# Kernel optimization log

Hardware: AMD Instinct MI355X
Metric: run time of the kernel (lower is better)

## Reference

```python
import jax, jax.numpy as jnp
import numpy as np

B, S, E, H, ML = 4, 1024, 1024, 16, 2048
HD = E // H


def setup_inputs() -> dict:
    key = jax.random.key(0)
    ks = jax.random.split(key, 8)
    s = 0.02
    return {
        "x": jax.random.normal(ks[0], (B, S, E), dtype=jnp.float32),
        "rel_pos": jax.random.normal(ks[1], (H, ML), dtype=jnp.float32),
        "in_proj_w": jax.random.normal(ks[2], (3 * E, E), dtype=jnp.float32) * s,
        "in_proj_b": jnp.zeros((3 * E,), jnp.float32),
        "out_w": jax.random.normal(ks[3], (E, E), dtype=jnp.float32) * s,
        "out_b": jnp.zeros((E,), jnp.float32),
        "w1": jax.random.normal(ks[4], (4 * E, E), dtype=jnp.float32) * s,
        "b1": jnp.zeros((4 * E,), jnp.float32),
        "w2": jax.random.normal(ks[5], (E, 4 * E), dtype=jnp.float32) * s,
        "b2": jnp.zeros((E,), jnp.float32),
        "ln1_g": jnp.ones((E,), jnp.float32),
        "ln1_b": jnp.zeros((E,), jnp.float32),
        "ln2_g": jnp.ones((E,), jnp.float32),
        "ln2_b": jnp.zeros((E,), jnp.float32),
    }


def _layernorm(x, g, b, eps=1e-5):
    m = x.mean(-1, keepdims=True)
    v = ((x - m) ** 2).mean(-1, keepdims=True)
    return (x - m) * jax.lax.rsqrt(v + eps) * g + b


def _causal_mask(size, rel_pos):
    # rel_pos: [H, max_len]; size <= max_len branch of the torch code
    flipped = jnp.flip(rel_pos[:, :size], -1)                        # [H, size]
    neg_inf = jnp.full((rel_pos.shape[0], size), -jnp.inf, rel_pos.dtype)
    padded = jnp.concatenate([flipped, neg_inf], axis=-1)            # [H, 2*size]
    idx = jnp.arange(size)[None, :] - jnp.arange(size)[:, None] + size - 1
    return padded[:, idx]                                            # [H, S, S]: rel_pos[i-j] if j<=i else -inf


def reference(x, rel_pos, in_proj_w, in_proj_b, out_w, out_b,
              w1, b1, w2, b2, ln1_g, ln1_b, ln2_g, ln2_b):
    b, s, e = x.shape
    xn = _layernorm(x, ln1_g, ln1_b)
    qkv = xn @ in_proj_w.T + in_proj_b                               # [B,S,3E]
    q, k, v = jnp.split(qkv, 3, axis=-1)
    q = q.reshape(b, s, H, HD).transpose(0, 2, 1, 3)                 # [B,H,S,D]
    k = k.reshape(b, s, H, HD).transpose(0, 2, 1, 3)
    v = v.reshape(b, s, H, HD).transpose(0, 2, 1, 3)
    mask = _causal_mask(s, rel_pos)                                  # [H,S,S], broadcast over batch (== repeat(B,1,1))
    scores = jnp.einsum("bhqd,bhkd->bhqk", q, k) / np.sqrt(HD) + mask[None]
    attn = jax.nn.softmax(scores, axis=-1)
    o = jnp.einsum("bhqk,bhkd->bhqd", attn, v)                       # [B,H,S,D]
    o = o.transpose(0, 2, 1, 3).reshape(b, s, e)
    att_out = o @ out_w.T + out_b
    x = x + att_out
    xm = _layernorm(x, ln2_g, ln2_b)
    mlp = jax.nn.relu(xm @ w1.T + b1) @ w2.T + b2
    return x + mlp
```

## Files before the change

kernel.cpp:

```cpp
#include <hip/hip_runtime.h>
#include <stdint.h>

typedef __bf16 bf16x8 __attribute__((ext_vector_type(8)));
typedef float  f32x4  __attribute__((ext_vector_type(4)));

__device__ __forceinline__ unsigned short f2bf(float f) {
  union { float f; unsigned int u; } a; a.f = f;
  unsigned int r = a.u + 0x7FFFu + ((a.u >> 16) & 1u);
  return (unsigned short)(r >> 16);
}

__device__ __forceinline__ unsigned short f2bf_fast(float f) {
  union { __bf16 b; unsigned short u; } v; v.b = (__bf16)f; return v.u;
}

__device__ __forceinline__ void cp16(const void* g, void* l) {
  auto g1 = reinterpret_cast<__attribute__((address_space(1))) unsigned int*>(
      reinterpret_cast<uintptr_t>(g));
  auto l3 = reinterpret_cast<__attribute__((address_space(3))) unsigned int*>(
      reinterpret_cast<uintptr_t>(l));
  __builtin_amdgcn_global_load_lds(g1, l3, 16, 0, 0);
}

__global__ __launch_bounds__(256) void cvt_all(
    const float* __restrict__ s0, const float* __restrict__ s1,
    const float* __restrict__ s2, const float* __restrict__ s3,
    unsigned short* __restrict__ d0, unsigned short* __restrict__ d1,
    unsigned short* __restrict__ d2, unsigned short* __restrict__ d3) {
  int i = (blockIdx.x * 256 + threadIdx.x) * 4;
  const float* src; unsigned short* dst; int off;
  if (i < 3145728)       { src = s0; dst = d0; off = 0; }
  else if (i < 4194304)  { src = s1; dst = d1; off = 3145728; }
  else if (i < 8388608)  { src = s2; dst = d2; off = 4194304; }
  else                   { src = s3; dst = d3; off = 8388608; }
  i -= off;
  float4 v = *(const float4*)(src + i);
  union { unsigned short u[4]; uint2 p; } o;
  o.u[0] = f2bf(v.x); o.u[1] = f2bf(v.y); o.u[2] = f2bf(v.z); o.u[3] = f2bf(v.w);
  *(uint2*)(dst + i) = o.p;
}

__global__ __launch_bounds__(256) void ln_bf16_seed(
    const float* __restrict__ x,
    const float* __restrict__ g,
    const float* __restrict__ bta,
    unsigned short* __restrict__ out,
    const float* __restrict__ seed_bias,
    float* __restrict__ seed_out) {
  const int row = blockIdx.x, t = threadIdx.x;
  const float4 v = *(const float4*)(x + (size_t)row * 1024 + t * 4);
  {
    float4 sb = *(const float4*)(seed_bias + t * 4);
    float4 sv;
    sv.x = v.x + sb.x; sv.y = v.y + sb.y; sv.z = v.z + sb.z; sv.w = v.w + sb.w;
    *(float4*)(seed_out + (size_t)row * 1024 + t * 4) = sv;
  }
  float s1 = v.x + v.y + v.z + v.w;
  float s2 = v.x*v.x + v.y*v.y + v.z*v.z + v.w*v.w;
  #pragma unroll
  for (int off = 1; off < 64; off <<= 1) {
    s1 += __shfl_xor(s1, off, 64);
    s2 += __shfl_xor(s2, off, 64);
  }
  __shared__ float r1[4], r2[4];
  if ((t & 63) == 0) { r1[t >> 6] = s1; r2[t >> 6] = s2; }
  __syncthreads();
  s1 = r1[0] + r1[1] + r1[2] + r1[3];
  s2 = r2[0] + r2[1] + r2[2] + r2[3];
  const float mean = s1 * (1.0f / 1024.0f);
  const float var  = s2 * (1.0f / 1024.0f) - mean * mean;
  const float rstd = rsqrtf(var + 1e-5f);
  const float4 gv = *(const float4*)(g + t * 4);
  const float4 bv = *(const float4*)(bta + t * 4);
  union { unsigned short u[4]; uint2 p; } o;
  o.u[0] = f2bf((v.x - mean) * rstd * gv.x + bv.x);
  o.u[1] = f2bf((v.y - mean) * rstd * gv.y + bv.y);
  o.u[2] = f2bf((v.z - mean) * rstd * gv.z + bv.z);
  o.u[3] = f2bf((v.w - mean) * rstd * gv.w + bv.w);
  *(uint2*)(out + (size_t)row * 1024 + t * 4) = o.p;
}

template <int MODE>
__device__ __forceinline__ void gemm_core(
    const unsigned short* __restrict__ A,
    const unsigned short* __restrict__ Bt,
    const float* __restrict__ bias,
    void* __restrict__ outp,
    int N, int K, int kbeg, int kend,
    unsigned short* As, unsigned short* Bs) {
  const int tid = threadIdx.x;
  const int wave = tid >> 6, lane = tid & 63;
  const int q = lane >> 4, c = lane & 15;
  const int wm = (wave & 1) << 6, wn = (wave >> 1) << 6;
  const int m0 = blockIdx.x << 7, n0 = blockIdx.y << 7;

  const int srow = tid >> 3;
  const int cg8  = ((tid & 7) ^ (srow & 7)) << 3;

  const unsigned short* gA = A  + (size_t)(m0 + srow) * K + cg8;
  const unsigned short* gB = Bt + (size_t)(n0 + srow) * K + cg8;
  const size_t rstep = (size_t)32 * K;

  auto issue = [&](int k0, int buf) {
    unsigned short* lA = As + buf * 8192 + tid * 8;
    unsigned short* lB = Bs + buf * 8192 + tid * 8;
    #pragma unroll
    for (int it = 0; it < 4; it++) {
      cp16(gA + it * rstep + k0, lA + it * 2048);
      cp16(gB + it * rstep + k0, lB + it * 2048);
    }
  };

  const f32x4 fzero = {0.f, 0.f, 0.f, 0.f};
  f32x4 acc[4][4];
  #pragma unroll
  for (int i = 0; i < 4; i++)
    #pragma unroll
    for (int j = 0; j < 4; j++) acc[i][j] = fzero;

  issue(kbeg, 0);
  if (kbeg + 64 < kend) issue(kbeg + 64, 1);

  int buf = 0;
  for (int k0 = kbeg; k0 < kend; k0 += 64, buf ^= 1) {
    if (k0 + 64 < kend) asm volatile("s_waitcnt vmcnt(8)" ::: "memory");
    else                asm volatile("s_waitcnt vmcnt(0)" ::: "memory");
    asm volatile("s_barrier" ::: "memory");

    const unsigned short* cA = As + buf * 8192;
    const unsigned short* cB = Bs + buf * 8192;
    #pragma unroll
    for (int ks = 0; ks < 2; ks++) {
      const int sw = (((ks << 2) + q) ^ (c & 7)) << 3;
      bf16x8 af[4], bf[4];
      #pragma unroll
      for (int i = 0; i < 4; i++) af[i] = *(const bf16x8*)&cA[(wm + i*16 + c)*64 + sw];
      #pragma unroll
      for (int j = 0; j < 4; j++) bf[j] = *(const bf16x8*)&cB[(wn + j*16 + c)*64 + sw];
      #pragma unroll
      for (int i = 0; i < 4; i++)
        #pragma unroll
        for (int j = 0; j < 4; j++)
          acc[i][j] = __builtin_amdgcn_mfma_f32_16x16x32_bf16(af[i], bf[j], acc[i][j], 0, 0, 0);
    }

    asm volatile("s_barrier" ::: "memory");
    if (k0 + 128 < kend) issue(k0 + 128, buf);
  }

  if (MODE == 4) {
    float* op = (float*)outp;
    #pragma unroll
    for (int i = 0; i < 4; i++) {
      #pragma unroll
      for (int r = 0; r < 4; r++) {
        const int row = m0 + wm + i * 16 + q * 4 + r;
        #pragma unroll
        for (int j = 0; j < 4; j++) {
          const int col = n0 + wn + j * 16 + c;
          atomicAdd(op + (size_t)row * N + col, acc[i][j][r]);
        }
      }
    }
  } else {
    float bj[4];
    #pragma unroll
    for (int j = 0; j < 4; j++) bj[j] = bias[n0 + wn + j * 16 + c];
    #pragma unroll
    for (int i = 0; i < 4; i++) {
      #pragma unroll
      for (int r = 0; r < 4; r++) {
        const int row = m0 + wm + i * 16 + q * 4 + r;
        #pragma unroll
        for (int j = 0; j < 4; j++) {
          const int col = n0 + wn + j * 16 + c;
          const size_t idx = (size_t)row * N + col;
          float v = acc[i][j][r] + bj[j];
          if (MODE == 0) ((unsigned short*)outp)[idx] = f2bf(v);
          else           ((unsigned short*)outp)[idx] = f2bf(fmaxf(v, 0.f));
        }
      }
    }
  }
}

template <int MODE>
__global__ __launch_bounds__(256, 2) void gemm_bt(
    const unsigned short* __restrict__ A,
    const unsigned short* __restrict__ Bt,
    const float* __restrict__ bias,
    void* __restrict__ outp,
    int N, int K) {
  __shared__ __align__(16) unsigned short As[2 * 128 * 64];
  __shared__ __align__(16) unsigned short Bs[2 * 128 * 64];
  gemm_core<MODE>(A, Bt, bias, outp, N, K, 0, K, As, Bs);
}

__global__ __launch_bounds__(256, 2) void gemm_bt_splitk(
    const unsigned short* __restrict__ A,
    const unsigned short* __restrict__ Bt,
    float* __restrict__ outp,
    int N, int K) {
  __shared__ __align__(16) unsigned short As[2 * 128 * 64];
  __shared__ __align__(16) unsigned short Bs[2 * 128 * 64];
  const int KH = K >> 1;
  const int kbeg = blockIdx.z * KH;
  gemm_core<4>(A, Bt, nullptr, outp, N, K, kbeg, kbeg + KH, As, Bs);
}

__global__ __launch_bounds__(256, 2) void attn_flash(
    const unsigned short* __restrict__ qkv,
    const float* __restrict__ rel_pos,
    unsigned short* __restrict__ o) {
  __shared__ __align__(16) unsigned short Qs[128 * 64];
  __shared__ __align__(16) unsigned short Ks[64 * 64];
  __shared__ __align__(16) unsigned short Vs[64 * 64];
  __shared__ __align__(16) unsigned short Ps[4][32 * 64];
  __shared__ float rps[1024];

  const int tid = threadIdx.x;
  const int wave = tid >> 6, lane = tid & 63;
  const int q = lane >> 4, c = lane & 15;

  const int lid = blockIdx.x + (blockIdx.y << 3);
  const int xq = lid & 7, y = lid >> 3;
  const int qt = (y & 32) ? (7 - xq) : xq;
  const int b = y >> 4, h = y & 15;

  const unsigned short* qg = qkv + (size_t)b * 1024 * 3072 + h * 64;
  const unsigned short* kg = qg + 1024;
  const unsigned short* vg = qg + 2048;

  #pragma unroll
  for (int i = 0; i < 4; i++) {
    const int idx = tid + i * 256;
    rps[idx & 1023] = rel_pos[h * 2048 + (idx & 1023)] * 1.44269504f;
  }

  const int sr  = tid >> 3;
  const int cg8 = ((tid & 7) ^ (sr & 7)) << 3;
  #pragma unroll
  for (int it = 0; it < 4; it++)
    cp16(qg + (size_t)(qt * 128 + sr + it * 32) * 3072 + cg8, &Qs[(tid + it * 256) * 8]);
  __syncthreads();

  bf16x8 qf[2][2];
  #pragma unroll
  for (int mt = 0; mt < 2; mt++)
    #pragma unroll
    for (int ks = 0; ks < 2; ks++)
      qf[mt][ks] = *(const bf16x8*)&Qs[(wave*32 + mt*16 + c)*64 + ((((ks<<2)+q) ^ (c & 7)) << 3)];

  const f32x4 fzero = {0.f, 0.f, 0.f, 0.f};
  f32x4 O[2][4];
  float l_i[2][4];
  #pragma unroll
  for (int mt = 0; mt < 2; mt++) {
    #pragma unroll
    for (int r = 0; r < 4; r++) l_i[mt][r] = 0.f;
    #pragma unroll
    for (int dt = 0; dt < 4; dt++) O[mt][dt] = fzero;
  }

  unsigned short* Pw = &Ps[wave][0];
  const int i_base = qt * 128 + wave * 32;
  const int vrow = tid & 63, d0 = (tid >> 6) << 4;
  const int vchunk = vrow >> 3, vlo = vrow & 7;

  const float sc = 0.125f * 1.44269504f;
  const int kdiag = qt << 1;
  const int nkt = (qt + 1) * 2;

  for (int kt = 0; kt < nkt; kt++) {
    __syncthreads();
    cp16(kg + (size_t)(kt * 64 + sr) * 3072 + cg8, &Ks[tid * 8]);
    cp16(kg + (size_t)(kt * 64 + sr + 32) * 3072 + cg8, &Ks[(tid + 256) * 8]);
    {
      union { int4 v; unsigned short u[8]; } va, vb2;
      const unsigned short* vrp = vg + (size_t)(kt * 64 + vrow) * 3072 + d0;
      va.v  = *(const int4*)vrp;
      vb2.v = *(const int4*)(vrp + 8);
      #pragma unroll
      for (int j = 0; j < 8; j++) {
        const int pos = ((vchunk ^ j) << 3) + vlo;
        Vs[(d0 + j) * 64 + pos]     = va.u[j];
        Vs[(d0 + 8 + j) * 64 + pos] = vb2.u[j];
      }
    }
    __syncthreads();

    f32x4 S[2][4];
    #pragma unroll
    for (int mt = 0; mt < 2; mt++)
      #pragma unroll
      for (int nt = 0; nt < 4; nt++) S[mt][nt] = fzero;
    #pragma unroll
    for (int ks = 0; ks < 2; ks++) {
      const int sw = (((ks << 2) + q) ^ (c & 7)) << 3;
      bf16x8 kb[4];
      #pragma unroll
      for (int nt = 0; nt < 4; nt++) kb[nt] = *(const bf16x8*)&Ks[(nt*16 + c)*64 + sw];
      #pragma unroll
      for (int mt = 0; mt < 2; mt++)
        #pragma unroll
        for (int nt = 0; nt < 4; nt++)
          S[mt][nt] = __builtin_amdgcn_mfma_f32_16x16x32_bf16(qf[mt][ks], kb[nt], S[mt][nt], 0, 0, 0);
    }

    if (kt < kdiag) {
      #pragma unroll
      for (int mt = 0; mt < 2; mt++) {
        #pragma unroll
        for (int r = 0; r < 4; r++) {
          const int i_ = i_base + mt * 16 + q * 4 + r;
          const int prow = (mt * 16 + q * 4 + r) * 64;
          const int rsw  = (q * 4 + r) & 7;
          float s = 0.f;
          #pragma unroll
          for (int nt = 0; nt < 4; nt++) {
            const int j_ = kt * 64 + nt * 16 + c;
            const float p = exp2f(fmaf(S[mt][nt][r], sc, rps[i_ - j_]));
            s += p;
            Pw[prow + ((((nt << 1) + (c >> 3)) ^ rsw) << 3) + (c & 7)] = f2bf_fast(p);
          }
          l_i[mt][r] += s;
        }
      }
    } else {
      #pragma unroll
      for (int mt = 0; mt < 2; mt++) {
        #pragma unroll
        for (int r = 0; r < 4; r++) {
          const int i_ = i_base + mt * 16 + q * 4 + r;
          const int prow = (mt * 16 + q * 4 + r) * 64;
          const int rsw  = (q * 4 + r) & 7;
          float s = 0.f;
          #pragma unroll
          for (int nt = 0; nt < 4; nt++) {
            const int j_ = kt * 64 + nt * 16 + c;
            const int d_ = i_ - j_;
            const float p = (d_ >= 0)
                ? exp2f(fmaf(S[mt][nt][r], sc, rps[d_ & 1023])) : 0.f;
            s += p;
            Pw[prow + ((((nt << 1) + (c >> 3)) ^ rsw) << 3) + (c & 7)] = f2bf_fast(p);
          }
          l_i[mt][r] += s;
        }
      }
    }

    asm volatile("s_waitcnt lgkmcnt(0)" ::: "memory");

    #pragma unroll
    for (int ks = 0; ks < 2; ks++) {
      const int sw = (((ks << 2) + q) ^ (c & 7)) << 3;
      bf16x8 pa[2], vb[4];
      #pragma unroll
      for (int mt = 0; mt < 2; mt++) pa[mt] = *(const bf16x8*)&Pw[(mt*16 + c)*64 + sw];
      #pragma unroll
      for (int dt = 0; dt < 4; dt++) vb[dt] = *(const bf16x8*)&Vs[(dt*16 + c)*64 + sw];
      #pragma unroll
      for (int mt = 0; mt < 2; mt++)
        #pragma unroll
        for (int dt = 0; dt < 4; dt++)
          O[mt][dt] = __builtin_amdgcn_mfma_f32_16x16x32_bf16(pa[mt], vb[dt], O[mt][dt], 0, 0, 0);
    }
  }

  #pragma unroll
  for (int mt = 0; mt < 2; mt++) {
    #pragma unroll
    for (int r = 0; r < 4; r++) {
      float l = l_i[mt][r];
      l += __shfl_xor(l, 1, 64);
      l += __shfl_xor(l, 2, 64);
      l += __shfl_xor(l, 4, 64);
      l += __shfl_xor(l, 8, 64);
      const float inv = 1.0f / l;
      const int i_ = i_base + mt * 16 + q * 4 + r;
      unsigned short* orow = o + (size_t)(b * 1024 + i_) * 1024 + h * 64 + c;
      #pragma unroll
      for (int dt = 0; dt < 4; dt++) orow[dt * 16] = f2bf(O[mt][dt][r] * inv);
    }
  }
}

extern "C" void kernel_launch(void* const* d_in, const int* in_sizes, int n_in,
                              void* d_out, int out_size, void* d_ws, size_t ws_size,
                              hipStream_t stream) {
  (void)in_sizes; (void)n_in; (void)out_size; (void)ws_size;
  const float* x    = (const float*)d_in[0];
  const float* rel  = (const float*)d_in[1];
  const float* ipw  = (const float*)d_in[2];
  const float* ipb  = (const float*)d_in[3];
  const float* outw = (const float*)d_in[4];
  const float* outb = (const float*)d_in[5];
  const float* w1   = (const float*)d_in[6];
  const float* b1   = (const float*)d_in[7];
  const float* w2   = (const float*)d_in[8];
  const float* b2   = (const float*)d_in[9];
  const float* ln1g = (const float*)d_in[10];
  const float* ln1b = (const float*)d_in[11];
  const float* ln2g = (const float*)d_in[12];
  const float* ln2b = (const float*)d_in[13];

  unsigned short* ipw_b  = (unsigned short*)d_ws;
  unsigned short* outw_b = ipw_b  + (size_t)3072 * 1024;
  unsigned short* w1_b   = outw_b + (size_t)1024 * 1024;
  unsigned short* w2_b   = w1_b   + (size_t)4096 * 1024;
  unsigned short* xn     = w2_b   + (size_t)1024 * 4096;
  unsigned short* qkvb   = xn     + (size_t)4096 * 1024;
  unsigned short* ob     = qkvb   + (size_t)4096 * 3072;
  float*          x2     = (float*)(ob + (size_t)4096 * 1024);
  unsigned short* xm     = (unsigned short*)(x2 + (size_t)4096 * 1024);
  unsigned short* hb     = xm + (size_t)4096 * 1024;

  cvt_all<<<12288, 256, 0, stream>>>(ipw, outw, w1, w2, ipw_b, outw_b, w1_b, w2_b);

  ln_bf16_seed<<<4096, 256, 0, stream>>>(x, ln1g, ln1b, xn, outb, x2);

  gemm_bt<0><<<dim3(32, 24), 256, 0, stream>>>(xn, ipw_b, ipb, qkvb, 3072, 1024);

  attn_flash<<<dim3(8, 64), 256, 0, stream>>>(qkvb, rel, ob);

  gemm_bt_splitk<<<dim3(32, 8, 2), 256, 0, stream>>>(ob, outw_b, x2, 1024, 1024);

  ln_bf16_seed<<<4096, 256, 0, stream>>>(x2, ln2g, ln2b, xm, b2, (float*)d_out);

  gemm_bt<2><<<dim3(32, 32), 256, 0, stream>>>(xm, w1_b, b1, hb, 4096, 1024);

  gemm_bt_splitk<<<dim3(32, 8, 2), 256, 0, stream>>>(hb, w2_b, (float*)d_out, 1024, 4096);
}
```

Baseline: 337.3 us.

## Deepen GEMM and attention load pipelines with smaller K tiles and prefetch

The GEMM core now uses 32-wide K tiles with a new swizzled LDS layout and a configurable ring of 2 or 3 buffers, so more loads are in flight. Occupancy hints are tuned per GEMM instance. The final down-projection uses a three-way split-K with a ragged chunk size. The attention kernel triple-buffers K in LDS via async copies and prefetches the next V tile into registers, replacing two full syncthreads per step with a waitcnt plus barrier scheme. The cost is more LDS, more register pressure and extra atomic traffic from the larger split-K.

```diff
diff --git a/kernel.cpp b/kernel.cpp
--- a/kernel.cpp
+++ b/kernel.cpp
@@ -80,7 +80,7 @@
   *(uint2*)(out + (size_t)row * 1024 + t * 4) = o.p;
 }
 
-template <int MODE>
+template <int MODE, int NBUF>
 __device__ __forceinline__ void gemm_core(
     const unsigned short* __restrict__ A,
     const unsigned short* __restrict__ Bt,
@@ -94,22 +94,28 @@
   const int wm = (wave & 1) << 6, wn = (wave >> 1) << 6;
   const int m0 = blockIdx.x << 7, n0 = blockIdx.y << 7;
 
-  const int srow = tid >> 3;
-  const int cg8  = ((tid & 7) ^ (srow & 7)) << 3;
-
-  const unsigned short* gA = A  + (size_t)(m0 + srow) * K + cg8;
-  const unsigned short* gB = Bt + (size_t)(n0 + srow) * K + cg8;
-  const size_t rstep = (size_t)32 * K;
-
-  auto issue = [&](int k0, int buf) {
-    unsigned short* lA = As + buf * 8192 + tid * 8;
-    unsigned short* lB = Bs + buf * 8192 + tid * 8;
-    #pragma unroll
-    for (int it = 0; it < 4; it++) {
-      cp16(gA + it * rstep + k0, lA + it * 2048);
-      cp16(gB + it * rstep + k0, lB + it * 2048);
-    }
+  const int row0 = ((tid >> 3) << 1) | ((tid >> 2) & 1);
+  const int gcol = ((tid & 3) ^ ((tid >> 3) & 3)) << 3;
+  const unsigned short* gA = A  + (size_t)(m0 + row0) * K + gcol + kbeg;
+  const unsigned short* gB = Bt + (size_t)(n0 + row0) * K + gcol + kbeg;
+  const size_t rstep64 = (size_t)64 * K;
+
+  const int nit = (kend - kbeg) >> 5;
+
+  auto issue = [&](int it) {
+    const int buf = it % NBUF;
+    const int k0 = it << 5;
+    unsigned short* lA = As + buf * 4096 + tid * 8;
+    unsigned short* lB = Bs + buf * 4096 + tid * 8;
+    cp16(gA + k0, lA);
+    cp16(gA + rstep64 + k0, lA + 2048);
+    cp16(gB + k0, lB);
+    cp16(gB + rstep64 + k0, lB + 2048);
   };
+
+  const int laneoff = ((c >> 1) << 6) + ((c & 1) << 5) + ((q ^ ((c >> 1) & 3)) << 3);
+  const int aoff = (wm << 5) + laneoff;
+  const int boff = (wn << 5) + laneoff;
 
   const f32x4 fzero = {0.f, 0.f, 0.f, 0.f};
   f32x4 acc[4][4];
@@ -118,34 +124,36 @@
     #pragma unroll
     for (int j = 0; j < 4; j++) acc[i][j] = fzero;
 
-  issue(kbeg, 0);
-  if (kbeg + 64 < kend) issue(kbeg + 64, 1);
-
-  int buf = 0;
-  for (int k0 = kbeg; k0 < kend; k0 += 64, buf ^= 1) {
-    if (k0 + 64 < kend) asm volatile("s_waitcnt vmcnt(8)" ::: "memory");
-    else                asm volatile("s_waitcnt vmcnt(0)" ::: "memory");
+  issue(0);
+  if (nit > 1) issue(1);
+  if (NBUF >= 3 && nit > 2) issue(2);
+
+  for (int it = 0; it < nit; ++it) {
+    if (NBUF >= 3) {
+      if (it + 2 < nit)      asm volatile("s_waitcnt vmcnt(8)" ::: "memory");
+      else if (it + 1 < nit) asm volatile("s_waitcnt vmcnt(4)" ::: "memory");
+      else                   asm volatile("s_waitcnt vmcnt(0)" ::: "memory");
+    } else {
+      if (it + 1 < nit) asm volatile("s_waitcnt vmcnt(4)" ::: "memory");
+      else              asm volatile("s_waitcnt vmcnt(0)" ::: "memory");
+    }
     asm volatile("s_barrier" ::: "memory");
 
-    const unsigned short* cA = As + buf * 8192;
-    const unsigned short* cB = Bs + buf * 8192;
-    #pragma unroll
-    for (int ks = 0; ks < 2; ks++) {
-      const int sw = (((ks << 2) + q) ^ (c & 7)) << 3;
-      bf16x8 af[4], bf[4];
-      #pragma unroll
-      for (int i = 0; i < 4; i++) af[i] = *(const bf16x8*)&cA[(wm + i*16 + c)*64 + sw];
-      #pragma unroll
-      for (int j = 0; j < 4; j++) bf[j] = *(const bf16x8*)&cB[(wn + j*16 + c)*64 + sw];
-      #pragma unroll
-      for (int i = 0; i < 4; i++)
-        #pragma unroll
-        for (int j = 0; j < 4; j++)
-          acc[i][j] = __builtin_amdgcn_mfma_f32_16x16x32_bf16(af[i], bf[j], acc[i][j], 0, 0, 0);
-    }
+    const unsigned short* cA = As + (it % NBUF) * 4096;
+    const unsigned short* cB = Bs + (it % NBUF) * 4096;
+    bf16x8 af[4], bf[4];
+    #pragma unroll
+    for (int i = 0; i < 4; i++) af[i] = *(const bf16x8*)&cA[aoff + i * 512];
+    #pragma unroll
+    for (int j = 0; j < 4; j++) bf[j] = *(const bf16x8*)&cB[boff + j * 512];
+    #pragma unroll
+    for (int i = 0; i < 4; i++)
+      #pragma unroll
+      for (int j = 0; j < 4; j++)
+        acc[i][j] = __builtin_amdgcn_mfma_f32_16x16x32_bf16(af[i], bf[j], acc[i][j], 0, 0, 0);
 
     asm volatile("s_barrier" ::: "memory");
-    if (k0 + 128 < kend) issue(k0 + 128, buf);
+    if (it + NBUF < nit) issue(it + NBUF);
   }
 
   if (MODE == 4) {
@@ -184,28 +192,29 @@
   }
 }
 
-template <int MODE>
-__global__ __launch_bounds__(256, 2) void gemm_bt(
+template <int MODE, int NBUF, int MINW>
+__global__ __launch_bounds__(256, MINW) void gemm_k(
     const unsigned short* __restrict__ A,
     const unsigned short* __restrict__ Bt,
     const float* __restrict__ bias,
     void* __restrict__ outp,
     int N, int K) {
-  __shared__ __align__(16) unsigned short As[2 * 128 * 64];
-  __shared__ __align__(16) unsigned short Bs[2 * 128 * 64];
-  gemm_core<MODE>(A, Bt, bias, outp, N, K, 0, K, As, Bs);
-}
-
-__global__ __launch_bounds__(256, 2) void gemm_bt_splitk(
+  __shared__ __align__(16) unsigned short As[NBUF * 4096];
+  __shared__ __align__(16) unsigned short Bs[NBUF * 4096];
+  gemm_core<MODE, NBUF>(A, Bt, bias, outp, N, K, 0, K, As, Bs);
+}
+
+template <int NBUF, int MINW>
+__global__ __launch_bounds__(256, MINW) void gemm_splitk(
     const unsigned short* __restrict__ A,
     const unsigned short* __restrict__ Bt,
     float* __restrict__ outp,
-    int N, int K) {
-  __shared__ __align__(16) unsigned short As[2 * 128 * 64];
-  __shared__ __align__(16) unsigned short Bs[2 * 128 * 64];
-  const int KH = K >> 1;
-  const int kbeg = blockIdx.z * KH;
-  gemm_core<4>(A, Bt, nullptr, outp, N, K, kbeg, kbeg + KH, As, Bs);
+    int N, int K, int CH) {
+  __shared__ __align__(16) unsigned short As[NBUF * 4096];
+  __shared__ __align__(16) unsigned short Bs[NBUF * 4096];
+  const int kbeg = blockIdx.z * CH;
+  int kend = kbeg + CH; if (kend > K) kend = K;
+  gemm_core<4, NBUF>(A, Bt, nullptr, outp, N, K, kbeg, kend, As, Bs);
 }
 
 __global__ __launch_bounds__(256, 2) void attn_flash(
@@ -213,8 +222,8 @@
     const float* __restrict__ rel_pos,
     unsigned short* __restrict__ o) {
   __shared__ __align__(16) unsigned short Qs[128 * 64];
-  __shared__ __align__(16) unsigned short Ks[64 * 64];
-  __shared__ __align__(16) unsigned short Vs[64 * 64];
+  __shared__ __align__(16) unsigned short Ks[3 * 64 * 64];
+  __shared__ __align__(16) unsigned short Vs[2 * 64 * 64];
   __shared__ __align__(16) unsigned short Ps[4][32 * 64];
   __shared__ float rps[1024];
 
@@ -271,24 +280,47 @@
   const int kdiag = qt << 1;
   const int nkt = (qt + 1) * 2;
 
+  union VReg { int4 v; unsigned short u[8]; };
+  VReg v0a, v0b, v1a, v1b;
+
+  auto issueK = [&](int kt) {
+    unsigned short* Kb = &Ks[(kt % 3) * 4096];
+    cp16(kg + (size_t)(kt * 64 + sr) * 3072 + cg8, Kb + tid * 8);
+    cp16(kg + (size_t)(kt * 64 + sr + 32) * 3072 + cg8, Kb + (tid + 256) * 8);
+  };
+
+  issueK(0);
+  {
+    const unsigned short* vrp = vg + (size_t)(0 * 64 + vrow) * 3072 + d0;
+    v0a.v = *(const int4*)vrp;
+    v0b.v = *(const int4*)(vrp + 8);
+  }
+  issueK(1);
+
   for (int kt = 0; kt < nkt; kt++) {
-    __syncthreads();
-    cp16(kg + (size_t)(kt * 64 + sr) * 3072 + cg8, &Ks[tid * 8]);
-    cp16(kg + (size_t)(kt * 64 + sr + 32) * 3072 + cg8, &Ks[(tid + 256) * 8]);
+    if (kt + 1 < nkt) {
+      const unsigned short* vrp = vg + (size_t)((kt + 1) * 64 + vrow) * 3072 + d0;
+      if (kt & 1) { v0a.v = *(const int4*)vrp; v0b.v = *(const int4*)(vrp + 8); }
+      else        { v1a.v = *(const int4*)vrp; v1b.v = *(const int4*)(vrp + 8); }
+    }
+    if (kt + 1 < nkt) asm volatile("s_waitcnt vmcnt(4)" ::: "memory");
+    else              asm volatile("s_waitcnt vmcnt(0)" ::: "memory");
+    asm volatile("s_barrier" ::: "memory");
+    if (kt + 2 < nkt) issueK(kt + 2);
+
     {
-      union { int4 v; unsigned short u[8]; } va, vb2;
-      const unsigned short* vrp = vg + (size_t)(kt * 64 + vrow) * 3072 + d0;
-      va.v  = *(const int4*)vrp;
-      vb2.v = *(const int4*)(vrp + 8);
+      unsigned short* Vb = &Vs[(kt & 1) * 4096];
+      const VReg& ra = (kt & 1) ? v1a : v0a;
+      const VReg& rb = (kt & 1) ? v1b : v0b;
       #pragma unroll
       for (int j = 0; j < 8; j++) {
         const int pos = ((vchunk ^ j) << 3) + vlo;
-        Vs[(d0 + j) * 64 + pos]     = va.u[j];
-        Vs[(d0 + 8 + j) * 64 + pos] = vb2.u[j];
+        Vb[(d0 + j) * 64 + pos]     = ra.u[j];
+        Vb[(d0 + 8 + j) * 64 + pos] = rb.u[j];
       }
     }
-    __syncthreads();
-
+
+    const unsigned short* Kb = &Ks[(kt % 3) * 4096];
     f32x4 S[2][4];
     #pragma unroll
     for (int mt = 0; mt < 2; mt++)
@@ -299,7 +331,7 @@
       const int sw = (((ks << 2) + q) ^ (c & 7)) << 3;
       bf16x8 kb[4];
       #pragma unroll
-      for (int nt = 0; nt < 4; nt++) kb[nt] = *(const bf16x8*)&Ks[(nt*16 + c)*64 + sw];
+      for (int nt = 0; nt < 4; nt++) kb[nt] = *(const bf16x8*)&Kb[(nt*16 + c)*64 + sw];
       #pragma unroll
       for (int mt = 0; mt < 2; mt++)
         #pragma unroll
@@ -350,7 +382,9 @@
     }
 
     asm volatile("s_waitcnt lgkmcnt(0)" ::: "memory");
-
+    asm volatile("s_barrier" ::: "memory");
+
+    const unsigned short* Vb = &Vs[(kt & 1) * 4096];
     #pragma unroll
     for (int ks = 0; ks < 2; ks++) {
       const int sw = (((ks << 2) + q) ^ (c & 7)) << 3;
@@ -358,7 +392,7 @@
       #pragma unroll
       for (int mt = 0; mt < 2; mt++) pa[mt] = *(const bf16x8*)&Pw[(mt*16 + c)*64 + sw];
       #pragma unroll
-      for (int dt = 0; dt < 4; dt++) vb[dt] = *(const bf16x8*)&Vs[(dt*16 + c)*64 + sw];
+      for (int dt = 0; dt < 4; dt++) vb[dt] = *(const bf16x8*)&Vb[(dt*16 + c)*64 + sw];
       #pragma unroll
       for (int mt = 0; mt < 2; mt++)
         #pragma unroll
@@ -419,15 +453,15 @@
 
   ln_bf16_seed<<<4096, 256, 0, stream>>>(x, ln1g, ln1b, xn, outb, x2);
 
-  gemm_bt<0><<<dim3(32, 24), 256, 0, stream>>>(xn, ipw_b, ipb, qkvb, 3072, 1024);
+  gemm_k<0, 3, 3><<<dim3(32, 24), 256, 0, stream>>>(xn, ipw_b, ipb, qkvb, 3072, 1024);
 
   attn_flash<<<dim3(8, 64), 256, 0, stream>>>(qkvb, rel, ob);
 
-  gemm_bt_splitk<<<dim3(32, 8, 2), 256, 0, stream>>>(ob, outw_b, x2, 1024, 1024);
+  gemm_splitk<3, 3><<<dim3(32, 8, 2), 256, 0, stream>>>(ob, outw_b, x2, 1024, 1024, 512);
 
   ln_bf16_seed<<<4096, 256, 0, stream>>>(x2, ln2g, ln2b, xm, b2, (float*)d_out);
 
-  gemm_bt<2><<<dim3(32, 32), 256, 0, stream>>>(xm, w1_b, b1, hb, 4096, 1024);
-
-  gemm_bt_splitk<<<dim3(32, 8, 2), 256, 0, stream>>>(hb, w2_b, (float*)d_out, 1024, 4096);
-}
+  gemm_k<2, 2, 4><<<dim3(32, 32), 256, 0, stream>>>(xm, w1_b, b1, hb, 4096, 1024);
+
+  gemm_splitk<3, 3><<<dim3(32, 8, 3), 256, 0, stream>>>(hb, w2_b, (float*)d_out, 1024, 4096, 1376);
+}
```

Result: slower. 384.8 us (+14.1%).

## Pre-swizzle weights into MFMA fragment layout and stream B straight to registers

Applied to the files above, without the earlier changes.

The weight conversion kernel now writes bf16 weights tiled into 64x64 blocks in the exact per-lane MFMA fragment order. The GEMM core can then load B fragments directly from global memory into registers, with one-iteration register prefetch, and no longer stages B through LDS. This halves LDS use per block, so launch bounds rise to 3 blocks per CU, and removes B LDS reads and bank traffic. Split-K for the output and second MLP projections goes from 2 to 3 chunks, using the new chunk-size parameter. The trade-off is duplicated global/L2 reads of B across waves that share a column tile, more registers for the double-buffered fragments, and extra atomic traffic from the third split.

```diff
diff --git a/kernel.cpp b/kernel.cpp
--- a/kernel.cpp
+++ b/kernel.cpp
@@ -22,22 +22,43 @@
   __builtin_amdgcn_global_load_lds(g1, l3, 16, 0, 0);
 }
 
-__global__ __launch_bounds__(256) void cvt_all(
-    const float* __restrict__ s0, const float* __restrict__ s1,
-    const float* __restrict__ s2, const float* __restrict__ s3,
-    unsigned short* __restrict__ d0, unsigned short* __restrict__ d1,
-    unsigned short* __restrict__ d2, unsigned short* __restrict__ d3) {
-  int i = (blockIdx.x * 256 + threadIdx.x) * 4;
-  const float* src; unsigned short* dst; int off;
-  if (i < 3145728)       { src = s0; dst = d0; off = 0; }
-  else if (i < 4194304)  { src = s1; dst = d1; off = 3145728; }
-  else if (i < 8388608)  { src = s2; dst = d2; off = 4194304; }
-  else                   { src = s3; dst = d3; off = 8388608; }
-  i -= off;
-  float4 v = *(const float4*)(src + i);
-  union { unsigned short u[4]; uint2 p; } o;
-  o.u[0] = f2bf(v.x); o.u[1] = f2bf(v.y); o.u[2] = f2bf(v.z); o.u[3] = f2bf(v.w);
-  *(uint2*)(dst + i) = o.p;
+__global__ __launch_bounds__(256) void cvt_frag(
+    const float* __restrict__ ipw, const float* __restrict__ outw,
+    const float* __restrict__ w1, const float* __restrict__ w2,
+    unsigned short* __restrict__ f_ipw, unsigned short* __restrict__ f_outw,
+    unsigned short* __restrict__ f_w1, unsigned short* __restrict__ f_w2) {
+  __shared__ unsigned short Ls[64][72];
+  const int b = blockIdx.x;
+  const float* src; unsigned short* dst; int Kt, local;
+  if (b < 768)       { src = ipw;  dst = f_ipw;  Kt = 16; local = b; }
+  else if (b < 1024) { src = outw; dst = f_outw; Kt = 16; local = b - 768; }
+  else if (b < 2048) { src = w1;   dst = f_w1;   Kt = 16; local = b - 1024; }
+  else               { src = w2;   dst = f_w2;   Kt = 64; local = b - 2048; }
+  const int tn = local / Kt, tk = local % Kt;
+  const int K = Kt << 6;
+  const int t = threadIdx.x;
+  const int r = t >> 2, cb = (t & 3) << 4;
+  const float* gp = src + (size_t)(tn * 64 + r) * K + tk * 64 + cb;
+  #pragma unroll
+  for (int u = 0; u < 4; u++) {
+    float4 v = *(const float4*)(gp + u * 4);
+    Ls[r][cb + u*4 + 0] = f2bf(v.x);
+    Ls[r][cb + u*4 + 1] = f2bf(v.y);
+    Ls[r][cb + u*4 + 2] = f2bf(v.z);
+    Ls[r][cb + u*4 + 3] = f2bf(v.w);
+  }
+  __syncthreads();
+  unsigned short* tile_dst = dst + (size_t)(tn * Kt + tk) * 4096;
+  #pragma unroll
+  for (int u = 0; u < 2; u++) {
+    const int cid = t + u * 256;
+    const int lane = cid & 63, j = (cid >> 6) & 3, ks = cid >> 8;
+    const int row = j * 16 + (lane & 15), col = ks * 32 + (lane >> 4) * 8;
+    union { unsigned short u16[8]; uint4 v; } o;
+    #pragma unroll
+    for (int e = 0; e < 8; e++) o.u16[e] = Ls[row][col + e];
+    *(uint4*)(tile_dst + cid * 8) = o.v;
+  }
 }
 
 __global__ __launch_bounds__(256) void ln_bf16_seed(
@@ -83,11 +104,11 @@
 template <int MODE>
 __device__ __forceinline__ void gemm_core(
     const unsigned short* __restrict__ A,
-    const unsigned short* __restrict__ Bt,
+    const unsigned short* __restrict__ Bf,
     const float* __restrict__ bias,
     void* __restrict__ outp,
     int N, int K, int kbeg, int kend,
-    unsigned short* As, unsigned short* Bs) {
+    unsigned short* As) {
   const int tid = threadIdx.x;
   const int wave = tid >> 6, lane = tid & 63;
   const int q = lane >> 4, c = lane & 15;
@@ -96,19 +117,30 @@
 
   const int srow = tid >> 3;
   const int cg8  = ((tid & 7) ^ (srow & 7)) << 3;
-
-  const unsigned short* gA = A  + (size_t)(m0 + srow) * K + cg8;
-  const unsigned short* gB = Bt + (size_t)(n0 + srow) * K + cg8;
+  const unsigned short* gA = A + (size_t)(m0 + srow) * K + cg8 + kbeg;
   const size_t rstep = (size_t)32 * K;
 
-  auto issue = [&](int k0, int buf) {
-    unsigned short* lA = As + buf * 8192 + tid * 8;
-    unsigned short* lB = Bs + buf * 8192 + tid * 8;
-    #pragma unroll
-    for (int it = 0; it < 4; it++) {
-      cp16(gA + it * rstep + k0, lA + it * 2048);
-      cp16(gB + it * rstep + k0, lB + it * 2048);
-    }
+  const int Kt = K >> 6;
+  const int nt64 = (blockIdx.y << 1) + (wave >> 1);
+  const unsigned short* gBw = Bf + (size_t)(nt64 * Kt + (kbeg >> 6)) * 4096 + lane * 8;
+
+  const int nit = (kend - kbeg) >> 6;
+
+  auto issueA = [&](int it) {
+    unsigned short* lA = As + (it & 1) * 8192 + tid * 8;
+    const unsigned short* g = gA + ((size_t)it << 6);
+    cp16(g, lA);
+    cp16(g + rstep,     lA + 2048);
+    cp16(g + 2 * rstep, lA + 4096);
+    cp16(g + 3 * rstep, lA + 6144);
+  };
+  auto loadB = [&](int it, bf16x8 (&dst)[2][4]) {
+    const unsigned short* bt = gBw + (size_t)it * 4096;
+    #pragma unroll
+    for (int ks = 0; ks < 2; ks++)
+      #pragma unroll
+      for (int j = 0; j < 4; j++)
+        dst[ks][j] = *(const bf16x8*)(bt + (ks * 4 + j) * 512);
   };
 
   const f32x4 fzero = {0.f, 0.f, 0.f, 0.f};
@@ -118,34 +150,39 @@
     #pragma unroll
     for (int j = 0; j < 4; j++) acc[i][j] = fzero;
 
-  issue(kbeg, 0);
-  if (kbeg + 64 < kend) issue(kbeg + 64, 1);
-
-  int buf = 0;
-  for (int k0 = kbeg; k0 < kend; k0 += 64, buf ^= 1) {
-    if (k0 + 64 < kend) asm volatile("s_waitcnt vmcnt(8)" ::: "memory");
-    else                asm volatile("s_waitcnt vmcnt(0)" ::: "memory");
+  bf16x8 bcur[2][4], bnext[2][4];
+
+  issueA(0);
+  loadB(0, bcur);
+  if (nit > 1) issueA(1);
+
+  auto body = [&](int it, bf16x8 (&bc)[2][4], bf16x8 (&bn)[2][4]) {
+    if (it + 1 < nit) asm volatile("s_waitcnt vmcnt(12)" ::: "memory");
+    else              asm volatile("s_waitcnt vmcnt(8)"  ::: "memory");
     asm volatile("s_barrier" ::: "memory");
-
-    const unsigned short* cA = As + buf * 8192;
-    const unsigned short* cB = Bs + buf * 8192;
+    if (it + 1 < nit) loadB(it + 1, bn);
+
+    const unsigned short* cA = As + (it & 1) * 8192;
     #pragma unroll
     for (int ks = 0; ks < 2; ks++) {
       const int sw = (((ks << 2) + q) ^ (c & 7)) << 3;
-      bf16x8 af[4], bf[4];
+      bf16x8 af[4];
       #pragma unroll
       for (int i = 0; i < 4; i++) af[i] = *(const bf16x8*)&cA[(wm + i*16 + c)*64 + sw];
       #pragma unroll
-      for (int j = 0; j < 4; j++) bf[j] = *(const bf16x8*)&cB[(wn + j*16 + c)*64 + sw];
-      #pragma unroll
       for (int i = 0; i < 4; i++)
         #pragma unroll
         for (int j = 0; j < 4; j++)
-          acc[i][j] = __builtin_amdgcn_mfma_f32_16x16x32_bf16(af[i], bf[j], acc[i][j], 0, 0, 0);
+          acc[i][j] = __builtin_amdgcn_mfma_f32_16x16x32_bf16(af[i], bc[ks][j], acc[i][j], 0, 0, 0);
     }
 
     asm volatile("s_barrier" ::: "memory");
-    if (k0 + 128 < kend) issue(k0 + 128, buf);
+    if (it + 2 < nit) issueA(it + 2);
+  };
+
+  for (int it = 0; it < nit; it += 2) {
+    body(it,     bcur, bnext);
+    body(it + 1, bnext, bcur);
   }
 
   if (MODE == 4) {
@@ -185,27 +222,25 @@
 }
 
 template <int MODE>
-__global__ __launch_bounds__(256, 2) void gemm_bt(
+__global__ __launch_bounds__(256, 3) void gemm_f(
     const unsigned short* __restrict__ A,
-    const unsigned short* __restrict__ Bt,
+    const unsigned short* __restrict__ Bf,
     const float* __restrict__ bias,
     void* __restrict__ outp,
     int N, int K) {
-  __shared__ __align__(16) unsigned short As[2 * 128 * 64];
-  __shared__ __align__(16) unsigned short Bs[2 * 128 * 64];
-  gemm_core<MODE>(A, Bt, bias, outp, N, K, 0, K, As, Bs);
-}
-
-__global__ __launch_bounds__(256, 2) void gemm_bt_splitk(
+  __shared__ __align__(16) unsigned short As[2 * 8192];
+  gemm_core<MODE>(A, Bf, bias, outp, N, K, 0, K, As);
+}
+
+__global__ __launch_bounds__(256, 3) void gemm_f_splitk(
     const unsigned short* __restrict__ A,
-    const unsigned short* __restrict__ Bt,
+    const unsigned short* __restrict__ Bf,
     float* __restrict__ outp,
-    int N, int K) {
-  __shared__ __align__(16) unsigned short As[2 * 128 * 64];
-  __shared__ __align__(16) unsigned short Bs[2 * 128 * 64];
-  const int KH = K >> 1;
-  const int kbeg = blockIdx.z * KH;
-  gemm_core<4>(A, Bt, nullptr, outp, N, K, kbeg, kbeg + KH, As, Bs);
+    int N, int K, int CH) {
+  __shared__ __align__(16) unsigned short As[2 * 8192];
+  const int kbeg = blockIdx.z * CH;
+  int kend = kbeg + CH; if (kend > K) kend = K;
+  gemm_core<4>(A, Bf, nullptr, outp, N, K, kbeg, kend, As);
 }
 
 __global__ __launch_bounds__(256, 2) void attn_flash(
@@ -404,30 +439,30 @@
   const float* ln2g = (const float*)d_in[12];
   const float* ln2b = (const float*)d_in[13];
 
-  unsigned short* ipw_b  = (unsigned short*)d_ws;
-  unsigned short* outw_b = ipw_b  + (size_t)3072 * 1024;
-  unsigned short* w1_b   = outw_b + (size_t)1024 * 1024;
-  unsigned short* w2_b   = w1_b   + (size_t)4096 * 1024;
-  unsigned short* xn     = w2_b   + (size_t)1024 * 4096;
+  unsigned short* f_ipw  = (unsigned short*)d_ws;
+  unsigned short* f_outw = f_ipw  + (size_t)3072 * 1024;
+  unsigned short* f_w1   = f_outw + (size_t)1024 * 1024;
+  unsigned short* f_w2   = f_w1   + (size_t)4096 * 1024;
+  unsigned short* xn     = f_w2   + (size_t)1024 * 4096;
   unsigned short* qkvb   = xn     + (size_t)4096 * 1024;
   unsigned short* ob     = qkvb   + (size_t)4096 * 3072;
   float*          x2     = (float*)(ob + (size_t)4096 * 1024);
   unsigned short* xm     = (unsigned short*)(x2 + (size_t)4096 * 1024);
   unsigned short* hb     = xm + (size_t)4096 * 1024;
 
-  cvt_all<<<12288, 256, 0, stream>>>(ipw, outw, w1, w2, ipw_b, outw_b, w1_b, w2_b);
+  cvt_frag<<<3072, 256, 0, stream>>>(ipw, outw, w1, w2, f_ipw, f_outw, f_w1, f_w2);
 
   ln_bf16_seed<<<4096, 256, 0, stream>>>(x, ln1g, ln1b, xn, outb, x2);
 
-  gemm_bt<0><<<dim3(32, 24), 256, 0, stream>>>(xn, ipw_b, ipb, qkvb, 3072, 1024);
+  gemm_f<0><<<dim3(32, 24), 256, 0, stream>>>(xn, f_ipw, ipb, qkvb, 3072, 1024);
 
   attn_flash<<<dim3(8, 64), 256, 0, stream>>>(qkvb, rel, ob);
 
-  gemm_bt_splitk<<<dim3(32, 8, 2), 256, 0, stream>>>(ob, outw_b, x2, 1024, 1024);
+  gemm_f_splitk<<<dim3(32, 8, 3), 256, 0, stream>>>(ob, f_outw, x2, 1024, 1024, 384);
 
   ln_bf16_seed<<<4096, 256, 0, stream>>>(x2, ln2g, ln2b, xm, b2, (float*)d_out);
 
-  gemm_bt<2><<<dim3(32, 32), 256, 0, stream>>>(xm, w1_b, b1, hb, 4096, 1024);
-
-  gemm_bt_splitk<<<dim3(32, 8, 2), 256, 0, stream>>>(hb, w2_b, (float*)d_out, 1024, 4096);
-}
+  gemm_f<2><<<dim3(32, 32), 256, 0, stream>>>(xm, f_w1, b1, hb, 4096, 1024);
+
+  gemm_f_splitk<<<dim3(32, 8, 3), 256, 0, stream>>>(hb, f_w2, (float*)d_out, 1024, 4096, 1408);
+}
```

New measurement: 405.9 us. 20.4% more time.

## Single-buffer GEMM B tile for 3-block occupancy, fuse cvt+LN1, split-K 3

Applied to the files above, without the earlier changes.

The GEMM core now keeps the A tile double-buffered but loads the B tile into a single LDS buffer. This cuts shared memory per block enough to raise the launch bound to 3 blocks per CU. The catch is that the B load for the next step is issued only after the current step's compute and waited on right away, so part of its latency is exposed and has to be hidden by the extra occupancy. The weight-conversion kernel and the first layernorm are merged into one launch to save a launch and a sync point. The final MLP down-projection moves from a 2-way to a 3-way split-K with uneven chunks, to fill more CUs at the cost of more atomic adds.

```diff
diff --git a/kernel.cpp b/kernel.cpp
--- a/kernel.cpp
+++ b/kernel.cpp
@@ -22,22 +22,62 @@
   __builtin_amdgcn_global_load_lds(g1, l3, 16, 0, 0);
 }
 
-__global__ __launch_bounds__(256) void cvt_all(
+__global__ __launch_bounds__(256) void cvt_ln1(
     const float* __restrict__ s0, const float* __restrict__ s1,
     const float* __restrict__ s2, const float* __restrict__ s3,
     unsigned short* __restrict__ d0, unsigned short* __restrict__ d1,
-    unsigned short* __restrict__ d2, unsigned short* __restrict__ d3) {
-  int i = (blockIdx.x * 256 + threadIdx.x) * 4;
-  const float* src; unsigned short* dst; int off;
-  if (i < 3145728)       { src = s0; dst = d0; off = 0; }
-  else if (i < 4194304)  { src = s1; dst = d1; off = 3145728; }
-  else if (i < 8388608)  { src = s2; dst = d2; off = 4194304; }
-  else                   { src = s3; dst = d3; off = 8388608; }
-  i -= off;
-  float4 v = *(const float4*)(src + i);
+    unsigned short* __restrict__ d2, unsigned short* __restrict__ d3,
+    const float* __restrict__ x,
+    const float* __restrict__ g,
+    const float* __restrict__ bta,
+    unsigned short* __restrict__ out,
+    const float* __restrict__ seed_bias,
+    float* __restrict__ seed_out) {
+  if (blockIdx.x < 12288) {
+    int i = (blockIdx.x * 256 + threadIdx.x) * 4;
+    const float* src; unsigned short* dst; int off;
+    if (i < 3145728)       { src = s0; dst = d0; off = 0; }
+    else if (i < 4194304)  { src = s1; dst = d1; off = 3145728; }
+    else if (i < 8388608)  { src = s2; dst = d2; off = 4194304; }
+    else                   { src = s3; dst = d3; off = 8388608; }
+    i -= off;
+    float4 v = *(const float4*)(src + i);
+    union { unsigned short u[4]; uint2 p; } o;
+    o.u[0] = f2bf(v.x); o.u[1] = f2bf(v.y); o.u[2] = f2bf(v.z); o.u[3] = f2bf(v.w);
+    *(uint2*)(dst + i) = o.p;
+    return;
+  }
+  const int row = blockIdx.x - 12288, t = threadIdx.x;
+  const float4 v = *(const float4*)(x + (size_t)row * 1024 + t * 4);
+  {
+    float4 sb = *(const float4*)(seed_bias + t * 4);
+    float4 sv;
+    sv.x = v.x + sb.x; sv.y = v.y + sb.y; sv.z = v.z + sb.z; sv.w = v.w + sb.w;
+    *(float4*)(seed_out + (size_t)row * 1024 + t * 4) = sv;
+  }
+  float s1v = v.x + v.y + v.z + v.w;
+  float s2v = v.x*v.x + v.y*v.y + v.z*v.z + v.w*v.w;
+  #pragma unroll
+  for (int off = 1; off < 64; off <<= 1) {
+    s1v += __shfl_xor(s1v, off, 64);
+    s2v += __shfl_xor(s2v, off, 64);
+  }
+  __shared__ float r1[4], r2[4];
+  if ((t & 63) == 0) { r1[t >> 6] = s1v; r2[t >> 6] = s2v; }
+  __syncthreads();
+  s1v = r1[0] + r1[1] + r1[2] + r1[3];
+  s2v = r2[0] + r2[1] + r2[2] + r2[3];
+  const float mean = s1v * (1.0f / 1024.0f);
+  const float var  = s2v * (1.0f / 1024.0f) - mean * mean;
+  const float rstd = rsqrtf(var + 1e-5f);
+  const float4 gv = *(const float4*)(g + t * 4);
+  const float4 bv = *(const float4*)(bta + t * 4);
   union { unsigned short u[4]; uint2 p; } o;
-  o.u[0] = f2bf(v.x); o.u[1] = f2bf(v.y); o.u[2] = f2bf(v.z); o.u[3] = f2bf(v.w);
-  *(uint2*)(dst + i) = o.p;
+  o.u[0] = f2bf((v.x - mean) * rstd * gv.x + bv.x);
+  o.u[1] = f2bf((v.y - mean) * rstd * gv.y + bv.y);
+  o.u[2] = f2bf((v.z - mean) * rstd * gv.z + bv.z);
+  o.u[3] = f2bf((v.w - mean) * rstd * gv.w + bv.w);
+  *(uint2*)(out + (size_t)row * 1024 + t * 4) = o.p;
 }
 
 __global__ __launch_bounds__(256) void ln_bf16_seed(
@@ -87,7 +127,8 @@
     const float* __restrict__ bias,
     void* __restrict__ outp,
     int N, int K, int kbeg, int kend,
-    unsigned short* As, unsigned short* Bs) {
+    unsigned short* As,
+    unsigned short* Bs) {
   const int tid = threadIdx.x;
   const int wave = tid >> 6, lane = tid & 63;
   const int q = lane >> 4, c = lane & 15;
@@ -97,18 +138,27 @@
   const int srow = tid >> 3;
   const int cg8  = ((tid & 7) ^ (srow & 7)) << 3;
 
-  const unsigned short* gA = A  + (size_t)(m0 + srow) * K + cg8;
-  const unsigned short* gB = Bt + (size_t)(n0 + srow) * K + cg8;
+  const unsigned short* gA = A  + (size_t)(m0 + srow) * K + cg8 + kbeg;
+  const unsigned short* gB = Bt + (size_t)(n0 + srow) * K + cg8 + kbeg;
   const size_t rstep = (size_t)32 * K;
 
-  auto issue = [&](int k0, int buf) {
-    unsigned short* lA = As + buf * 8192 + tid * 8;
-    unsigned short* lB = Bs + buf * 8192 + tid * 8;
-    #pragma unroll
-    for (int it = 0; it < 4; it++) {
-      cp16(gA + it * rstep + k0, lA + it * 2048);
-      cp16(gB + it * rstep + k0, lB + it * 2048);
-    }
+  const int nit = (kend - kbeg) >> 6;
+
+  auto issueA = [&](int it) {
+    unsigned short* lA = As + (it & 1) * 8192 + tid * 8;
+    const unsigned short* g = gA + ((size_t)it << 6);
+    cp16(g,             lA);
+    cp16(g + rstep,     lA + 2048);
+    cp16(g + 2 * rstep, lA + 4096);
+    cp16(g + 3 * rstep, lA + 6144);
+  };
+  auto issueB = [&](int it) {
+    unsigned short* lB = Bs + tid * 8;
+    const unsigned short* g = gB + ((size_t)it << 6);
+    cp16(g,             lB);
+    cp16(g + rstep,     lB + 2048);
+    cp16(g + 2 * rstep, lB + 4096);
+    cp16(g + 3 * rstep, lB + 6144);
   };
 
   const f32x4 fzero = {0.f, 0.f, 0.f, 0.f};
@@ -118,17 +168,16 @@
     #pragma unroll
     for (int j = 0; j < 4; j++) acc[i][j] = fzero;
 
-  issue(kbeg, 0);
-  if (kbeg + 64 < kend) issue(kbeg + 64, 1);
-
-  int buf = 0;
-  for (int k0 = kbeg; k0 < kend; k0 += 64, buf ^= 1) {
-    if (k0 + 64 < kend) asm volatile("s_waitcnt vmcnt(8)" ::: "memory");
-    else                asm volatile("s_waitcnt vmcnt(0)" ::: "memory");
+  issueA(0);
+  issueB(0);
+  if (nit > 1) issueA(1);
+
+  for (int it = 0; it < nit; ++it) {
+    if (it + 1 < nit) asm volatile("s_waitcnt vmcnt(4)" ::: "memory");
+    else              asm volatile("s_waitcnt vmcnt(0)" ::: "memory");
     asm volatile("s_barrier" ::: "memory");
 
-    const unsigned short* cA = As + buf * 8192;
-    const unsigned short* cB = Bs + buf * 8192;
+    const unsigned short* cA = As + (it & 1) * 8192;
     #pragma unroll
     for (int ks = 0; ks < 2; ks++) {
       const int sw = (((ks << 2) + q) ^ (c & 7)) << 3;
@@ -136,7 +185,7 @@
       #pragma unroll
       for (int i = 0; i < 4; i++) af[i] = *(const bf16x8*)&cA[(wm + i*16 + c)*64 + sw];
       #pragma unroll
-      for (int j = 0; j < 4; j++) bf[j] = *(const bf16x8*)&cB[(wn + j*16 + c)*64 + sw];
+      for (int j = 0; j < 4; j++) bf[j] = *(const bf16x8*)&Bs[(wn + j*16 + c)*64 + sw];
       #pragma unroll
       for (int i = 0; i < 4; i++)
         #pragma unroll
@@ -145,7 +194,8 @@
     }
 
     asm volatile("s_barrier" ::: "memory");
-    if (k0 + 128 < kend) issue(k0 + 128, buf);
+    if (it + 1 < nit) issueB(it + 1);
+    if (it + 2 < nit) issueA(it + 2);
   }
 
   if (MODE == 4) {
@@ -185,27 +235,27 @@
 }
 
 template <int MODE>
-__global__ __launch_bounds__(256, 2) void gemm_bt(
+__global__ __launch_bounds__(256, 3) void gemm_s(
     const unsigned short* __restrict__ A,
     const unsigned short* __restrict__ Bt,
     const float* __restrict__ bias,
     void* __restrict__ outp,
     int N, int K) {
-  __shared__ __align__(16) unsigned short As[2 * 128 * 64];
-  __shared__ __align__(16) unsigned short Bs[2 * 128 * 64];
+  __shared__ __align__(16) unsigned short As[2 * 8192];
+  __shared__ __align__(16) unsigned short Bs[8192];
   gemm_core<MODE>(A, Bt, bias, outp, N, K, 0, K, As, Bs);
 }
 
-__global__ __launch_bounds__(256, 2) void gemm_bt_splitk(
+__global__ __launch_bounds__(256, 3) void gemm_s_splitk(
     const unsigned short* __restrict__ A,
     const unsigned short* __restrict__ Bt,
     float* __restrict__ outp,
-    int N, int K) {
-  __shared__ __align__(16) unsigned short As[2 * 128 * 64];
-  __shared__ __align__(16) unsigned short Bs[2 * 128 * 64];
-  const int KH = K >> 1;
-  const int kbeg = blockIdx.z * KH;
-  gemm_core<4>(A, Bt, nullptr, outp, N, K, kbeg, kbeg + KH, As, Bs);
+    int N, int K, int CH) {
+  __shared__ __align__(16) unsigned short As[2 * 8192];
+  __shared__ __align__(16) unsigned short Bs[8192];
+  const int kbeg = blockIdx.z * CH;
+  int kend = kbeg + CH; if (kend > K) kend = K;
+  gemm_core<4>(A, Bt, nullptr, outp, N, K, kbeg, kend, As, Bs);
 }
 
 __global__ __launch_bounds__(256, 2) void attn_flash(
@@ -415,19 +465,18 @@
   unsigned short* xm     = (unsigned short*)(x2 + (size_t)4096 * 1024);
   unsigned short* hb     = xm + (size_t)4096 * 1024;
 
-  cvt_all<<<12288, 256, 0, stream>>>(ipw, outw, w1, w2, ipw_b, outw_b, w1_b, w2_b);
-
-  ln_bf16_seed<<<4096, 256, 0, stream>>>(x, ln1g, ln1b, xn, outb, x2);
-
-  gemm_bt<0><<<dim3(32, 24), 256, 0, stream>>>(xn, ipw_b, ipb, qkvb, 3072, 1024);
+  cvt_ln1<<<16384, 256, 0, stream>>>(ipw, outw, w1, w2, ipw_b, outw_b, w1_b, w2_b,
+                                     x, ln1g, ln1b, xn, outb, x2);
+
+  gemm_s<0><<<dim3(32, 24), 256, 0, stream>>>(xn, ipw_b, ipb, qkvb, 3072, 1024);
 
   attn_flash<<<dim3(8, 64), 256, 0, stream>>>(qkvb, rel, ob);
 
-  gemm_bt_splitk<<<dim3(32, 8, 2), 256, 0, stream>>>(ob, outw_b, x2, 1024, 1024);
+  gemm_s_splitk<<<dim3(32, 8, 2), 256, 0, stream>>>(ob, outw_b, x2, 1024, 1024, 512);
 
   ln_bf16_seed<<<4096, 256, 0, stream>>>(x2, ln2g, ln2b, xm, b2, (float*)d_out);
 
-  gemm_bt<2><<<dim3(32, 32), 256, 0, stream>>>(xm, w1_b, b1, hb, 4096, 1024);
-
-  gemm_bt_splitk<<<dim3(32, 8, 2), 256, 0, stream>>>(hb, w2_b, (float*)d_out, 1024, 4096);
-}
+  gemm_s<2><<<dim3(32, 32), 256, 0, stream>>>(xm, w1_b, b1, hb, 4096, 1024);
+
+  gemm_s_splitk<<<dim3(32, 8, 3), 256, 0, stream>>>(hb, w2_b, (float*)d_out, 1024, 4096, 1408);
+}
```

Measured after the change: 348.2 us. 3.2% more time.
